# Kernel optimization log

Hardware: AMD Instinct MI355X
Metric: run time of the kernel (lower is better)

## Reference

```python
import jax, jax.numpy as jnp
import numpy as np

B, C, H, W = 8, 256, 64, 64
NH = 8
CM = 2048
EPS = 1e-5


def setup_inputs() -> dict:
    key = jax.random.key(0)
    ks = jax.random.split(key, 16)
    n = lambda k, s: (jax.random.normal(k, s, dtype=jnp.float32) * 0.02)
    return {
        'x': jax.random.normal(ks[0], (B, C, H, W), dtype=jnp.float32),
        'Wqkv': n(ks[1], (C, 3 * C)), 'bqkv': n(ks[2], (3 * C,)),
        'dw_w': n(ks[3], (C, 1, 3, 3)), 'dw_b': n(ks[4], (C,)),
        'Wproj': n(ks[5], (C, C)), 'bproj': n(ks[6], (C,)),
        'bn1_g': jnp.ones((C,), jnp.float32), 'bn1_b': jnp.zeros((C,), jnp.float32),
        'bn1_m': n(ks[7], (C,)), 'bn1_v': jax.random.uniform(ks[8], (C,), dtype=jnp.float32) + 0.5,
        'alpha1': jnp.ones((1,), jnp.float32),
        'Wfc1': n(ks[9], (C, CM)), 'bfc1': n(ks[10], (CM,)),
        'Wfc2': n(ks[11], (CM, C)), 'bfc2': n(ks[12], (C,)),
        'bn2_g': jnp.ones((C,), jnp.float32), 'bn2_b': jnp.zeros((C,), jnp.float32),
        'bn2_m': n(ks[13], (C,)), 'bn2_v': jax.random.uniform(ks[14], (C,), dtype=jnp.float32) + 0.5,
        'alpha2': jnp.ones((1,), jnp.float32),
    }


def _repbn(x, g, b, m, v, alpha):
    # eval-mode RepBN: BatchNorm1d with running stats over channel dim + alpha*x
    bn = (x - m) * jax.lax.rsqrt(v + EPS) * g + b
    return bn + alpha * x


def reference(x, Wqkv, bqkv, dw_w, dw_b, Wproj, bproj,
              bn1_g, bn1_b, bn1_m, bn1_v, alpha1,
              Wfc1, bfc1, Wfc2, bfc2,
              bn2_g, bn2_b, bn2_m, bn2_v, alpha2):
    b, c, h, w = x.shape
    n = h * w
    hd = c // NH
    scale = hd ** (-0.5)
    t = x.reshape(b, c, n).transpose(0, 2, 1)  # [B,N,C]

    # --- SimplifiedLinearAttention ---
    qkv = (t @ Wqkv + bqkv).reshape(b, n, 3, NH, hd).transpose(2, 0, 3, 1, 4)
    q, k, v = qkv[0], qkv[1], qkv[2]          # [B,H,N,hd]
    q = jax.nn.relu(q) * scale
    k = jax.nn.relu(k)
    ctx = jnp.einsum('bhnd,bhne->bhde', k, v)  # [B,H,hd,hd] small context
    out = jnp.einsum('bhnd,bhde->bhne', q, ctx)
    out = out.transpose(0, 2, 1, 3).reshape(b, n, c)
    img = out.transpose(0, 2, 1).reshape(b, c, h, w)
    img = jax.lax.conv_general_dilated(img, dw_w, (1, 1), 'SAME',
                                       feature_group_count=c)
    img = img + dw_b[None, :, None, None]
    out = img.reshape(b, c, n).transpose(0, 2, 1)
    out = out @ Wproj + bproj

    # residual + RepBN (eval branch of LinearNorm)
    t = _repbn(t + out, bn1_g, bn1_b, bn1_m, bn1_v, alpha1)

    # FFN (exact GELU as nn.GELU default)
    ff = jax.nn.gelu(t @ Wfc1 + bfc1, approximate=False) @ Wfc2 + bfc2
    t = _repbn(t + ff, bn2_g, bn2_b, bn2_m, bn2_v, alpha2)

    return t.transpose(0, 2, 1).reshape(b, c, h, w)
```

## Files before the change

### kernel.cpp

```cpp
#include <hip/hip_runtime.h>
#include <hip/hip_bf16.h>
#include <math.h>

constexpr int B_ = 8, C_ = 256, H_ = 64, W_ = 64;
constexpr int N_ = H_ * W_;
constexpr int NH_ = 8;
constexpr int CM_ = 2048;
constexpr int M_ = B_ * N_;
constexpr float EPS_ = 1e-5f;

typedef __bf16 bf16_t;
typedef bf16_t bf16x8 __attribute__((ext_vector_type(8)));
typedef float f32x4 __attribute__((ext_vector_type(4)));

__device__ inline bf16_t f2b(float f) {
    __hip_bfloat16 h = __float2bfloat16(f);
    return *reinterpret_cast<bf16_t*>(&h);
}
__device__ inline float b2f(bf16_t b) {
    unsigned short u = *reinterpret_cast<unsigned short*>(&b);
    unsigned int x = (unsigned int)u << 16;
    return *reinterpret_cast<float*>(&x);
}

#define GLOAD_LDS16(gptr, lptr)                                                     \
    __builtin_amdgcn_global_load_lds(                                               \
        (const __attribute__((address_space(1))) void*)(gptr),                      \
        (__attribute__((address_space(3))) void*)(lptr), 16, 0, 0)

template <int MODE>
__global__ void transpose_cast(const void* __restrict__ in_, bf16_t* __restrict__ outb) {
    __shared__ float tile[32][33];
    int b  = blockIdx.z;
    int n0 = blockIdx.x * 32;
    int c0 = blockIdx.y * 32;
    int tx = threadIdx.x, ty = threadIdx.y;
#pragma unroll
    for (int i = ty; i < 32; i += 8) {
        size_t off = (size_t)b * C_ * N_ + (size_t)(c0 + i) * N_ + n0 + tx;
        tile[i][tx] = (MODE == 0) ? ((const float*)in_)[off] : b2f(((const bf16_t*)in_)[off]);
    }
    __syncthreads();
#pragma unroll
    for (int i = ty; i < 32; i += 8) {
        size_t off = (size_t)b * N_ * C_ + (size_t)(n0 + i) * C_ + c0 + tx;
        outb[off] = f2b(tile[tx][i]);
    }
}

__global__ void wcastT(const float* __restrict__ W, bf16_t* __restrict__ Wt,
                       int K, int N) {
    __shared__ float tile[32][33];
    int k0 = blockIdx.y * 32, n0 = blockIdx.x * 32;
    int tx = threadIdx.x, ty = threadIdx.y;
#pragma unroll
    for (int i = ty; i < 32; i += 8)
        tile[i][tx] = W[(size_t)(k0 + i) * N + n0 + tx];
    __syncthreads();
#pragma unroll
    for (int i = ty; i < 32; i += 8)
        Wt[(size_t)(n0 + i) * K + k0 + tx] = f2b(tile[tx][i]);
}

template <int EPI>
__global__ __launch_bounds__(256)
void gemm_bf16(const bf16_t* __restrict__ A, const bf16_t* __restrict__ Bt,
               const float* __restrict__ bias,
               float* __restrict__ Cf, bf16_t* __restrict__ Cb,
               int M, int N, int K,
               const bf16_t* __restrict__ tres_b,
               const float* __restrict__ g, const float* __restrict__ bb,
               const float* __restrict__ mm, const float* __restrict__ vv,
               const float* __restrict__ alpha, int row_off) {
    __shared__ bf16x8 ldsv[2048];
    char* lds = (char*)ldsv;

    int tid  = threadIdx.x;
    int lane = tid & 63;
    int w    = tid >> 6;
    int wm   = w >> 1, wn = w & 1;
    int brow = blockIdx.y * 128, bcol = blockIdx.x * 128;
    int rowl = lane & 15, kq = lane >> 4;

    f32x4 acc[4][4] = {};

    for (int k0 = 0; k0 < K; k0 += 64) {
#pragma unroll
        for (int j = 0; j < 4; ++j) {
            int jj = w * 4 + j;
            int msub = jj >> 1, kh = jj & 1;
            const bf16_t* ga = A + ((size_t)(brow + msub * 16 + rowl) * K + k0 + kh * 32 + kq * 8);
            GLOAD_LDS16(ga, lds + jj * 1024);
            const bf16_t* gb = Bt + ((size_t)(bcol + msub * 16 + rowl) * K + k0 + kh * 32 + kq * 8);
            GLOAD_LDS16(gb, lds + 16384 + jj * 1024);
        }
        __syncthreads();
#pragma unroll
        for (int ks = 0; ks < 2; ++ks) {
            bf16x8 af[4], bfr[4];
#pragma unroll
            for (int m = 0; m < 4; ++m) af[m] = ldsv[((wm * 4 + m) * 2 + ks) * 64 + lane];
#pragma unroll
            for (int n = 0; n < 4; ++n) bfr[n] = ldsv[1024 + ((wn * 4 + n) * 2 + ks) * 64 + lane];
#pragma unroll
            for (int m = 0; m < 4; ++m)
#pragma unroll
                for (int n = 0; n < 4; ++n)
                    acc[m][n] = __builtin_amdgcn_mfma_f32_16x16x32_bf16(af[m], bfr[n], acc[m][n], 0, 0, 0);
        }
        __syncthreads();
    }

    float alpha_v = (EPI == 1 || EPI == 3) ? alpha[0] : 0.f;
#pragma unroll
    for (int m = 0; m < 4; ++m) {
#pragma unroll
        for (int n = 0; n < 4; ++n) {
            int col = bcol + wn * 64 + n * 16 + (lane & 15);
            float bv = bias[col];
#pragma unroll
            for (int r = 0; r < 4; ++r) {
                int row = brow + wm * 64 + m * 16 + (lane >> 4) * 4 + r;
                float y = acc[m][n][r] + bv;
                if (EPI == 4) {
                    Cb[(size_t)row * N + col] = f2b(y);
                } else if (EPI == 2) {
                    float u = y * (0.7978845608f + 0.0356774081f * y * y);
                    float e = __expf(2.0f * u);
                    float ge = y - y * __builtin_amdgcn_rcpf(e + 1.0f);
                    Cb[(size_t)row * N + col] = f2b(ge);
                } else if (EPI == 1) {
                    float z = b2f(tres_b[(size_t)row * N + col]) + y;
                    float rr = (z - mm[col]) * rsqrtf(vv[col] + EPS_) * g[col] + bb[col] + alpha_v * z;
                    Cb[(size_t)row * N + col] = f2b(rr);
                } else {
                    int grow = row_off + row;
                    float z = b2f(tres_b[(size_t)grow * C_ + col]) + y;
                    float rr = (z - mm[col]) * rsqrtf(vv[col] + EPS_) * g[col] + bb[col] + alpha_v * z;
                    int bi = grow >> 12, ni = grow & (N_ - 1);
                    Cf[((size_t)bi * C_ + col) * N_ + ni] = rr;
                }
            }
        }
    }
}

__global__ void ctx_partial(const bf16_t* __restrict__ qkv, float* __restrict__ ctxp) {
    __shared__ float kb[64][40];
    __shared__ float vb[64][40];
    int seg = blockIdx.x;
    int bh  = blockIdx.y;
    int b = bh >> 3, h = bh & 7;
    int tid = threadIdx.x;
    int d  = tid >> 3;
    int e0 = (tid & 7) * 4;
    int lrow = tid >> 2, lcol = (tid & 3) * 8;
    float acc[4] = {0.f, 0.f, 0.f, 0.f};
    const size_t base = (size_t)b * N_ * 768 + h * 32;
    for (int n0 = seg * 512; n0 < seg * 512 + 512; n0 += 64) {
        size_t ra = base + (size_t)(n0 + lrow) * 768 + lcol;
        bf16x8 kv8 = *(const bf16x8*)(qkv + ra + 256);
        bf16x8 vv8 = *(const bf16x8*)(qkv + ra + 512);
#pragma unroll
        for (int j = 0; j < 8; ++j) {
            kb[lrow][lcol + j] = b2f(kv8[j]);
            vb[lrow][lcol + j] = b2f(vv8[j]);
        }
        __syncthreads();
#pragma unroll
        for (int nl = 0; nl < 64; ++nl) {
            float kv = fmaxf(kb[nl][d], 0.f);
#pragma unroll
            for (int j = 0; j < 4; ++j)
                acc[j] = fmaf(kv, vb[nl][e0 + j], acc[j]);
        }
        __syncthreads();
    }
    float* o = ctxp + ((size_t)seg * 64 + bh) * 1024 + d * 32 + e0;
#pragma unroll
    for (int j = 0; j < 4; ++j) o[j] = acc[j];
}

__global__ void ctx_reduce(const float* __restrict__ ctxp, float* __restrict__ ctx) {
    int idx = blockIdx.x * 256 + threadIdx.x;
    float s = 0.f;
#pragma unroll
    for (int seg = 0; seg < 8; ++seg) s += ctxp[(size_t)seg * 65536 + idx];
    ctx[idx] = s;
}

__global__ void attn_out(const bf16_t* __restrict__ qkv, const float* __restrict__ ctx,
                         bf16_t* __restrict__ img) {
    __shared__ float qb[64][33];
    __shared__ float cs[32][32];
    int n0 = blockIdx.x * 64;
    int bh = blockIdx.y;
    int b = bh >> 3, h = bh & 7;
    int tid = threadIdx.x;
    const float scale = 0.17677669529663687f;
    {
        float4 vv = ((const float4*)(ctx + (size_t)bh * 1024))[tid];
        ((float4*)&cs[0][0])[tid] = vv;
    }
    const size_t base = (size_t)b * N_ * 768 + h * 32;
    int lrow = tid >> 2, lcol = (tid & 3) * 8;
    {
        bf16x8 q8 = *(const bf16x8*)(qkv + base + (size_t)(n0 + lrow) * 768 + lcol);
#pragma unroll
        for (int j = 0; j < 8; ++j)
            qb[lrow][lcol + j] = fmaxf(b2f(q8[j]), 0.f) * scale;
    }
    __syncthreads();
    int nl = tid & 63, ebase = tid >> 6;
    bf16_t* outp = img + ((size_t)b * C_ + h * 32) * N_ + n0 + nl;
#pragma unroll
    for (int p = 0; p < 8; ++p) {
        int e = ebase + p * 4;
        float s = 0.f;
#pragma unroll
        for (int dd = 0; dd < 32; ++dd)
            s = fmaf(qb[nl][dd], cs[dd][e], s);
        outp[(size_t)e * N_] = f2b(s);
    }
}

__global__ __launch_bounds__(256)
void dwconv3x3(const bf16_t* __restrict__ img, const float* __restrict__ w,
               const float* __restrict__ bias, bf16_t* __restrict__ out) {
    __shared__ float sp[64][65];
    int bc = blockIdx.x;
    int c  = bc & 255;
    int tid = threadIdx.x;
    const bf16_t* ip = img + (size_t)bc * N_;
#pragma unroll
    for (int l = 0; l < 2; ++l) {
        int flat = (tid + l * 256) * 8;
        int row = flat >> 6, col = flat & 63;
        bf16x8 v8 = *(const bf16x8*)(ip + flat);
#pragma unroll
        for (int j = 0; j < 8; ++j) sp[row][col + j] = b2f(v8[j]);
    }
    float wv[9];
#pragma unroll
    for (int j = 0; j < 9; ++j) wv[j] = w[c * 9 + j];
    float bv = bias[c];
    __syncthreads();

    int y = tid >> 2, x0 = (tid & 3) * 16;
    float o[16];
#pragma unroll
    for (int i = 0; i < 16; ++i) o[i] = bv;
#pragma unroll
    for (int dy = -1; dy <= 1; ++dy) {
        int yy = y + dy;
        if (yy < 0 || yy > 63) continue;
#pragma unroll
        for (int dx = -1; dx <= 1; ++dx) {
            float wgt = wv[(dy + 1) * 3 + dx + 1];
#pragma unroll
            for (int i = 0; i < 16; ++i) {
                int xx = x0 + i + dx;
                float val = (xx < 0 || xx > 63) ? 0.f : sp[yy][xx];
                o[i] = fmaf(wgt, val, o[i]);
            }
        }
    }
    bf16_t ob[16];
#pragma unroll
    for (int i = 0; i < 16; ++i) ob[i] = f2b(o[i]);
    *(bf16x8*)(out + (size_t)bc * N_ + y * 64 + x0)     = *(bf16x8*)&ob[0];
    *(bf16x8*)(out + (size_t)bc * N_ + y * 64 + x0 + 8) = *(bf16x8*)&ob[8];
}

extern "C" void kernel_launch(void* const* d_in, const int* in_sizes, int n_in,
                              void* d_out, int out_size, void* d_ws, size_t ws_size,
                              hipStream_t stream) {
    const float* x     = (const float*)d_in[0];
    const float* Wqkv  = (const float*)d_in[1];
    const float* bqkv  = (const float*)d_in[2];
    const float* dw_w  = (const float*)d_in[3];
    const float* dw_b  = (const float*)d_in[4];
    const float* Wproj = (const float*)d_in[5];
    const float* bproj = (const float*)d_in[6];
    const float* bn1_g = (const float*)d_in[7];
    const float* bn1_b = (const float*)d_in[8];
    const float* bn1_m = (const float*)d_in[9];
    const float* bn1_v = (const float*)d_in[10];
    const float* alpha1= (const float*)d_in[11];
    const float* Wfc1  = (const float*)d_in[12];
    const float* bfc1  = (const float*)d_in[13];
    const float* Wfc2  = (const float*)d_in[14];
    const float* bfc2  = (const float*)d_in[15];
    const float* bn2_g = (const float*)d_in[16];
    const float* bn2_b = (const float*)d_in[17];
    const float* bn2_m = (const float*)d_in[18];
    const float* bn2_v = (const float*)d_in[19];
    const float* alpha2= (const float*)d_in[20];
    float* out = (float*)d_out;

    char* ws = (char*)d_ws;
    bf16_t* t_b2    = (bf16_t*)(ws);
    bf16_t* WqkvT   = (bf16_t*)(ws + 16777216);
    bf16_t* WprojT  = (bf16_t*)(ws + 17170432);
    bf16_t* Wfc1T   = (bf16_t*)(ws + 17301504);
    bf16_t* Wfc2T   = (bf16_t*)(ws + 18350080);
    float*  ctxp    = (float*)(ws + 19398656);
    float*  ctx     = (float*)(ws + 21495808);
    bf16_t* t_b     = (bf16_t*)(ws + 21757952);
    bf16_t* qkv_b   = (bf16_t*)(ws + 38535168);
    bf16_t* img_b   = (bf16_t*)(ws + 88866816);
    bf16_t* conv_b  = (bf16_t*)(ws + 105644032);
    bf16_t* convT_b = (bf16_t*)(ws + 122421248);
    bf16_t* hidden  = (bf16_t*)(ws + 21757952);

    transpose_cast<0><<<dim3(N_ / 32, C_ / 32, B_), dim3(32, 8), 0, stream>>>(x, t_b);
    wcastT<<<dim3(768 / 32, C_ / 32), dim3(32, 8), 0, stream>>>(Wqkv, WqkvT, C_, 768);
    wcastT<<<dim3(C_ / 32, C_ / 32), dim3(32, 8), 0, stream>>>(Wproj, WprojT, C_, C_);
    wcastT<<<dim3(CM_ / 32, C_ / 32), dim3(32, 8), 0, stream>>>(Wfc1, Wfc1T, C_, CM_);
    wcastT<<<dim3(C_ / 32, CM_ / 32), dim3(32, 8), 0, stream>>>(Wfc2, Wfc2T, CM_, C_);

    gemm_bf16<4><<<dim3(768 / 128, M_ / 128), 256, 0, stream>>>(
        t_b, WqkvT, bqkv, nullptr, qkv_b, M_, 768, C_,
        nullptr, nullptr, nullptr, nullptr, nullptr, nullptr, 0);

    ctx_partial<<<dim3(8, B_ * NH_), 256, 0, stream>>>(qkv_b, ctxp);
    ctx_reduce<<<256, 256, 0, stream>>>(ctxp, ctx);

    attn_out<<<dim3(N_ / 64, B_ * NH_), 256, 0, stream>>>(qkv_b, ctx, img_b);

    dwconv3x3<<<B_ * C_, 256, 0, stream>>>(img_b, dw_w, dw_b, conv_b);

    transpose_cast<1><<<dim3(N_ / 32, C_ / 32, B_), dim3(32, 8), 0, stream>>>(conv_b, convT_b);

    gemm_bf16<1><<<dim3(C_ / 128, M_ / 128), 256, 0, stream>>>(
        convT_b, WprojT, bproj, nullptr, t_b2, M_, C_, C_,
        t_b, bn1_g, bn1_b, bn1_m, bn1_v, alpha1, 0);

    gemm_bf16<2><<<dim3(CM_ / 128, M_ / 128), 256, 0, stream>>>(
        t_b2, Wfc1T, bfc1, nullptr, hidden, M_, CM_, C_,
        nullptr, nullptr, nullptr, nullptr, nullptr, nullptr, 0);

    gemm_bf16<3><<<dim3(C_ / 128, M_ / 128), 256, 0, stream>>>(
        hidden, Wfc2T, bfc2, out, nullptr, M_, C_, CM_,
        t_b2, bn2_g, bn2_b, bn2_m, bn2_v, alpha2, 0);
}
```

Before: 349.8 us.

## Fuse FFN fc1+GELU+fc2+RepBN into one kernel keeping hidden on-chip

Replaces the separate fc1 (GELU epilogue) and fc2 (RepBN epilogue) GEMMs with a single kernel in which each block holds 128 rows of activations in registers. The kernel streams 32-column chunks of W1 and W2 through double-buffered LDS, computes the GELU hidden chunk with 32x32 MFMAs, repacks it through lane shuffles and accumulates fc2 directly. This is meant to remove the 64 MB bf16 hidden tensor round trip through HBM and one launch. In exchange, grid size drops to 256 blocks, each block uses 128 KB of LDS so occupancy is low, and weights are reloaded per block with a sync on every chunk.

```diff
diff --git a/kernel.cpp b/kernel.cpp
--- a/kernel.cpp
+++ b/kernel.cpp
@@ -12,6 +12,8 @@
 typedef __bf16 bf16_t;
 typedef bf16_t bf16x8 __attribute__((ext_vector_type(8)));
 typedef float f32x4 __attribute__((ext_vector_type(4)));
+typedef float f32x16 __attribute__((ext_vector_type(16)));
+typedef unsigned int u32x4 __attribute__((ext_vector_type(4)));
 
 __device__ inline bf16_t f2b(float f) {
     __hip_bfloat16 h = __float2bfloat16(f);
@@ -21,6 +23,17 @@
     unsigned short u = *reinterpret_cast<unsigned short*>(&b);
     unsigned int x = (unsigned int)u << 16;
     return *reinterpret_cast<float*>(&x);
+}
+__device__ inline unsigned pk2(float lo, float hi) {
+    bf16_t l = f2b(lo), h = f2b(hi);
+    unsigned short ls = *reinterpret_cast<unsigned short*>(&l);
+    unsigned short hs = *reinterpret_cast<unsigned short*>(&h);
+    return ((unsigned)hs << 16) | (unsigned)ls;
+}
+__device__ inline float gelu_ap(float y) {
+    float u = y * (0.7978845608f + 0.0356774081f * y * y);
+    float e = __expf(2.0f * u);
+    return y - y * __builtin_amdgcn_rcpf(e + 1.0f);
 }
 
 #define GLOAD_LDS16(gptr, lptr)                                                     \
@@ -111,7 +124,7 @@
         __syncthreads();
     }
 
-    float alpha_v = (EPI == 1 || EPI == 3) ? alpha[0] : 0.f;
+    float alpha_v = (EPI == 1) ? alpha[0] : 0.f;
 #pragma unroll
     for (int m = 0; m < 4; ++m) {
 #pragma unroll
@@ -124,23 +137,138 @@
                 float y = acc[m][n][r] + bv;
                 if (EPI == 4) {
                     Cb[(size_t)row * N + col] = f2b(y);
-                } else if (EPI == 2) {
-                    float u = y * (0.7978845608f + 0.0356774081f * y * y);
-                    float e = __expf(2.0f * u);
-                    float ge = y - y * __builtin_amdgcn_rcpf(e + 1.0f);
-                    Cb[(size_t)row * N + col] = f2b(ge);
-                } else if (EPI == 1) {
+                } else {
                     float z = b2f(tres_b[(size_t)row * N + col]) + y;
                     float rr = (z - mm[col]) * rsqrtf(vv[col] + EPS_) * g[col] + bb[col] + alpha_v * z;
                     Cb[(size_t)row * N + col] = f2b(rr);
-                } else {
-                    int grow = row_off + row;
-                    float z = b2f(tres_b[(size_t)grow * C_ + col]) + y;
-                    float rr = (z - mm[col]) * rsqrtf(vv[col] + EPS_) * g[col] + bb[col] + alpha_v * z;
-                    int bi = grow >> 12, ni = grow & (N_ - 1);
-                    Cf[((size_t)bi * C_ + col) * N_ + ni] = rr;
                 }
             }
+        }
+    }
+}
+
+__global__ __launch_bounds__(256)
+void ffn_fused(const bf16_t* __restrict__ Aact, const bf16_t* __restrict__ W1t,
+               const bf16_t* __restrict__ W2t,
+               const float* __restrict__ bfc1, const float* __restrict__ bfc2,
+               const float* __restrict__ g, const float* __restrict__ bb,
+               const float* __restrict__ mm, const float* __restrict__ vv,
+               const float* __restrict__ alpha, float* __restrict__ out) {
+    __shared__ bf16x8 ldsv[8192];
+    char* lds = (char*)ldsv;
+    const int tid = threadIdx.x;
+    const int lane = tid & 63;
+    const int w = tid >> 6;
+    const int l31 = lane & 31;
+    const int h = lane >> 5;
+    const int brow = blockIdx.x * 128;
+
+    {
+        const bf16_t* ga = Aact + (size_t)(brow + 32 * w + l31) * 256 + h * 8;
+#pragma unroll
+        for (int kc = 0; kc < 16; ++kc)
+            GLOAD_LDS16(ga + kc * 16, lds + (w * 16 + kc) * 1024);
+        const bf16_t* g1 = W1t + (size_t)l31 * 256 + h * 8;
+#pragma unroll
+        for (int i = 0; i < 4; ++i) {
+            int kc = w * 4 + i;
+            GLOAD_LDS16(g1 + kc * 16, lds + 65536 + kc * 1024);
+        }
+#pragma unroll
+        for (int i = 0; i < 4; ++i) {
+            int fid = w * 4 + i, cb = fid >> 1, ks = fid & 1;
+            const bf16_t* g2 = W2t + (size_t)(32 * cb + l31) * 2048 + ks * 16 + h * 8;
+            GLOAD_LDS16(g2, lds + 98304 + fid * 1024);
+        }
+    }
+    __syncthreads();
+
+    bf16x8 areg[16];
+#pragma unroll
+    for (int kc = 0; kc < 16; ++kc) areg[kc] = ldsv[(w * 16 + kc) * 64 + lane];
+
+    f32x16 acc2[8];
+#pragma unroll
+    for (int cb = 0; cb < 8; ++cb) acc2[cb] = (f32x16)0.f;
+
+    const float* bp1 = bfc1 + 4 * h;
+
+    for (int c = 0; c < 64; ++c) {
+        int p = c & 1;
+        if (c + 1 < 64) {
+            int cn = c + 1, pn = p ^ 1;
+            const bf16_t* g1 = W1t + (size_t)(32 * cn + l31) * 256 + h * 8;
+#pragma unroll
+            for (int i = 0; i < 4; ++i) {
+                int kc = w * 4 + i;
+                GLOAD_LDS16(g1 + kc * 16, lds + 65536 + pn * 16384 + kc * 1024);
+            }
+#pragma unroll
+            for (int i = 0; i < 4; ++i) {
+                int fid = w * 4 + i, cb = fid >> 1, ks = fid & 1;
+                const bf16_t* g2 = W2t + (size_t)(32 * cb + l31) * 2048 + 32 * cn + ks * 16 + h * 8;
+                GLOAD_LDS16(g2, lds + 98304 + pn * 16384 + fid * 1024);
+            }
+        }
+
+        f32x16 acc1;
+#pragma unroll
+        for (int r = 0; r < 16; ++r)
+            acc1[r] = bp1[32 * c + (r & 3) + 8 * (r >> 2)];
+#pragma unroll
+        for (int kc = 0; kc < 16; ++kc) {
+            bf16x8 w1f = ldsv[4096 + p * 1024 + kc * 64 + lane];
+            acc1 = __builtin_amdgcn_mfma_f32_32x32x16_bf16(w1f, areg[kc], acc1, 0, 0, 0);
+        }
+
+        unsigned words[8];
+#pragma unroll
+        for (int t = 0; t < 4; ++t)
+#pragma unroll
+            for (int s = 0; s < 2; ++s)
+                words[t * 2 + s] = pk2(gelu_ap(acc1[4 * t + 2 * s]),
+                                       gelu_ap(acc1[4 * t + 2 * s + 1]));
+        bf16x8 hf[2];
+#pragma unroll
+        for (int ks = 0; ks < 2; ++ks) {
+            unsigned u0 = words[(2 * ks) * 2 + 0], u1 = words[(2 * ks) * 2 + 1];
+            unsigned v0 = words[(2 * ks + 1) * 2 + 0], v1 = words[(2 * ks + 1) * 2 + 1];
+            unsigned su0 = __shfl_xor(u0, 32);
+            unsigned su1 = __shfl_xor(u1, 32);
+            unsigned sv0 = __shfl_xor(v0, 32);
+            unsigned sv1 = __shfl_xor(v1, 32);
+            u32x4 t4;
+            t4[0] = h ? sv0 : u0;
+            t4[1] = h ? sv1 : u1;
+            t4[2] = h ? v0 : su0;
+            t4[3] = h ? v1 : su1;
+            hf[ks] = __builtin_bit_cast(bf16x8, t4);
+        }
+
+#pragma unroll
+        for (int cb = 0; cb < 8; ++cb) {
+            bf16x8 w2f0 = ldsv[6144 + p * 1024 + (cb * 2 + 0) * 64 + lane];
+            acc2[cb] = __builtin_amdgcn_mfma_f32_32x32x16_bf16(hf[0], w2f0, acc2[cb], 0, 0, 0);
+            bf16x8 w2f1 = ldsv[6144 + p * 1024 + (cb * 2 + 1) * 64 + lane];
+            acc2[cb] = __builtin_amdgcn_mfma_f32_32x32x16_bf16(hf[1], w2f1, acc2[cb], 0, 0, 0);
+        }
+        __syncthreads();
+    }
+
+    float alpha_v = alpha[0];
+#pragma unroll
+    for (int cb = 0; cb < 8; ++cb) {
+        int cc = cb * 32 + l31;
+        float bv = bfc2[cc];
+        float rs = rsqrtf(vv[cc] + EPS_) * g[cc];
+        float bbv = bb[cc], mv = mm[cc];
+#pragma unroll
+        for (int r = 0; r < 16; ++r) {
+            int m = brow + 32 * w + (r & 3) + 8 * (r >> 2) + 4 * h;
+            float z = b2f(Aact[(size_t)m * 256 + cc]) + acc2[cb][r] + bv;
+            float rr = (z - mv) * rs + bbv + alpha_v * z;
+            int bi = m >> 12, ni = m & (N_ - 1);
+            out[((size_t)bi * C_ + cc) * N_ + ni] = rr;
         }
     }
 }
@@ -311,7 +439,6 @@
     bf16_t* img_b   = (bf16_t*)(ws + 88866816);
     bf16_t* conv_b  = (bf16_t*)(ws + 105644032);
     bf16_t* convT_b = (bf16_t*)(ws + 122421248);
-    bf16_t* hidden  = (bf16_t*)(ws + 21757952);
 
     transpose_cast<0><<<dim3(N_ / 32, C_ / 32, B_), dim3(32, 8), 0, stream>>>(x, t_b);
     wcastT<<<dim3(768 / 32, C_ / 32), dim3(32, 8), 0, stream>>>(Wqkv, WqkvT, C_, 768);
@@ -336,11 +463,7 @@
         convT_b, WprojT, bproj, nullptr, t_b2, M_, C_, C_,
         t_b, bn1_g, bn1_b, bn1_m, bn1_v, alpha1, 0);
 
-    gemm_bf16<2><<<dim3(CM_ / 128, M_ / 128), 256, 0, stream>>>(
-        t_b2, Wfc1T, bfc1, nullptr, hidden, M_, CM_, C_,
-        nullptr, nullptr, nullptr, nullptr, nullptr, nullptr, 0);
-
-    gemm_bf16<3><<<dim3(C_ / 128, M_ / 128), 256, 0, stream>>>(
-        hidden, Wfc2T, bfc2, out, nullptr, M_, C_, CM_,
-        t_b2, bn2_g, bn2_b, bn2_m, bn2_v, alpha2, 0);
-}
+    ffn_fused<<<M_ / 128, 256, 0, stream>>>(
+        t_b2, Wfc1T, Wfc2T, bfc1, bfc2,
+        bn2_g, bn2_b, bn2_m, bn2_v, alpha2, out);
+}
```

New measurement: 377.9 us. 8.0% more time.

## Stage GEMM epilogue through LDS for vectorized stores and swizzle block order

Applied to the files above, without the earlier changes.

Rewrites the GEMM epilogue so bf16-output variants stage accumulators in a per-wave XOR-swizzled LDS buffer and write eight contiguous bf16 values per lane with vector loads of bias and BN parameters. The fp32 transposed-output variant writes four consecutive spatial positions per store instead of scalar scattered writes. It also remaps block indices with a stride-8 swizzle to change which tiles run together for L2 reuse. This targets uncoalesced 2-byte scattered stores in the epilogues, at the cost of LDS round-trips and reliance on explicit waitcnt ordering within each wave.

```diff
diff --git a/kernel.cpp b/kernel.cpp
--- a/kernel.cpp
+++ b/kernel.cpp
@@ -21,6 +21,11 @@
     unsigned short u = *reinterpret_cast<unsigned short*>(&b);
     unsigned int x = (unsigned int)u << 16;
     return *reinterpret_cast<float*>(&x);
+}
+__device__ inline float gelu_ap(float y) {
+    float u = y * (0.7978845608f + 0.0356774081f * y * y);
+    float e = __expf(2.0f * u);
+    return y - y * __builtin_amdgcn_rcpf(e + 1.0f);
 }
 
 #define GLOAD_LDS16(gptr, lptr)                                                     \
@@ -71,7 +76,7 @@
                const bf16_t* __restrict__ tres_b,
                const float* __restrict__ g, const float* __restrict__ bb,
                const float* __restrict__ mm, const float* __restrict__ vv,
-               const float* __restrict__ alpha, int row_off) {
+               const float* __restrict__ alpha) {
     __shared__ bf16x8 ldsv[2048];
     char* lds = (char*)ldsv;
 
@@ -79,7 +84,13 @@
     int lane = tid & 63;
     int w    = tid >> 6;
     int wm   = w >> 1, wn = w & 1;
-    int brow = blockIdx.y * 128, bcol = blockIdx.x * 128;
+
+    int nwg = gridDim.x * gridDim.y;
+    int bid = blockIdx.y * gridDim.x + blockIdx.x;
+    int swz = (bid & 7) * (nwg >> 3) + (bid >> 3);
+    int bx = swz % gridDim.x, by = swz / gridDim.x;
+    int brow = by * 128, bcol = bx * 128;
+
     int rowl = lane & 15, kq = lane >> 4;
 
     f32x4 acc[4][4] = {};
@@ -112,34 +123,86 @@
     }
 
     float alpha_v = (EPI == 1 || EPI == 3) ? alpha[0] : 0.f;
-#pragma unroll
-    for (int m = 0; m < 4; ++m) {
-#pragma unroll
-        for (int n = 0; n < 4; ++n) {
-            int col = bcol + wn * 64 + n * 16 + (lane & 15);
-            float bv = bias[col];
-#pragma unroll
-            for (int r = 0; r < 4; ++r) {
-                int row = brow + wm * 64 + m * 16 + (lane >> 4) * 4 + r;
-                float y = acc[m][n][r] + bv;
+
+    if (EPI == 3) {
+#pragma unroll
+        for (int m = 0; m < 4; ++m) {
+            int mbase = brow + wm * 64 + m * 16 + (lane >> 4) * 4;
+            int bi = mbase >> 12, ni = mbase & (N_ - 1);
+#pragma unroll
+            for (int n = 0; n < 4; ++n) {
+                int col = bcol + wn * 64 + n * 16 + (lane & 15);
+                float bv = bias[col];
+                float rs = rsqrtf(vv[col] + EPS_) * g[col];
+                float bbv = bb[col], mv = mm[col];
+                f32x4 o4;
+#pragma unroll
+                for (int r = 0; r < 4; ++r) {
+                    float z = b2f(tres_b[(size_t)(mbase + r) * C_ + col]) + acc[m][n][r] + bv;
+                    o4[r] = (z - mv) * rs + bbv + alpha_v * z;
+                }
+                *(f32x4*)(Cf + ((size_t)bi * C_ + col) * N_ + ni) = o4;
+            }
+        }
+    } else {
+        float* fl = (float*)ldsv + w * 2048;
+        const int c8 = lane & 7, rbase = (lane >> 3) * 4;
+#pragma unroll
+        for (int half = 0; half < 2; ++half) {
+            if (half)
+                asm volatile("s_waitcnt lgkmcnt(0)" ::: "memory");
+#pragma unroll
+            for (int m2 = 0; m2 < 2; ++m2) {
+                int m = half * 2 + m2;
+#pragma unroll
+                for (int n = 0; n < 4; ++n)
+#pragma unroll
+                    for (int r = 0; r < 4; ++r) {
+                        int rl = m2 * 16 + (lane >> 4) * 4 + r;
+                        int cl = n * 16 + (lane & 15);
+                        int scl = cl ^ (((rl >> 2) & 3) << 4);
+                        fl[rl * 64 + scl] = acc[m][n][r];
+                    }
+            }
+            asm volatile("s_waitcnt lgkmcnt(0)" ::: "memory");
+#pragma unroll
+            for (int rr = 0; rr < 4; ++rr) {
+                int rl = rbase + rr;
+                int xr = ((rl >> 2) & 3) << 4;
+                f32x4 lo = *(f32x4*)&fl[rl * 64 + ((c8 * 8) ^ xr)];
+                f32x4 hi = *(f32x4*)&fl[rl * 64 + ((c8 * 8 + 4) ^ xr)];
+                int grow = brow + wm * 64 + half * 32 + rl;
+                int gcol = bcol + wn * 64 + c8 * 8;
+                f32x4 b0 = *(const f32x4*)(bias + gcol);
+                f32x4 b1 = *(const f32x4*)(bias + gcol + 4);
+                float y[8];
+#pragma unroll
+                for (int j = 0; j < 4; ++j) { y[j] = lo[j] + b0[j]; y[4 + j] = hi[j] + b1[j]; }
+                bf16_t ob[8];
                 if (EPI == 4) {
-                    Cb[(size_t)row * N + col] = f2b(y);
+#pragma unroll
+                    for (int j = 0; j < 8; ++j) ob[j] = f2b(y[j]);
                 } else if (EPI == 2) {
-                    float u = y * (0.7978845608f + 0.0356774081f * y * y);
-                    float e = __expf(2.0f * u);
-                    float ge = y - y * __builtin_amdgcn_rcpf(e + 1.0f);
-                    Cb[(size_t)row * N + col] = f2b(ge);
-                } else if (EPI == 1) {
-                    float z = b2f(tres_b[(size_t)row * N + col]) + y;
-                    float rr = (z - mm[col]) * rsqrtf(vv[col] + EPS_) * g[col] + bb[col] + alpha_v * z;
-                    Cb[(size_t)row * N + col] = f2b(rr);
+#pragma unroll
+                    for (int j = 0; j < 8; ++j) ob[j] = f2b(gelu_ap(y[j]));
                 } else {
-                    int grow = row_off + row;
-                    float z = b2f(tres_b[(size_t)grow * C_ + col]) + y;
-                    float rr = (z - mm[col]) * rsqrtf(vv[col] + EPS_) * g[col] + bb[col] + alpha_v * z;
-                    int bi = grow >> 12, ni = grow & (N_ - 1);
-                    Cf[((size_t)bi * C_ + col) * N_ + ni] = rr;
+                    bf16x8 t8 = *(const bf16x8*)(tres_b + (size_t)grow * N + gcol);
+                    f32x4 g0 = *(const f32x4*)(g + gcol),  g1 = *(const f32x4*)(g + gcol + 4);
+                    f32x4 B0 = *(const f32x4*)(bb + gcol), B1 = *(const f32x4*)(bb + gcol + 4);
+                    f32x4 m0 = *(const f32x4*)(mm + gcol), m1 = *(const f32x4*)(mm + gcol + 4);
+                    f32x4 v0 = *(const f32x4*)(vv + gcol), v1 = *(const f32x4*)(vv + gcol + 4);
+#pragma unroll
+                    for (int j = 0; j < 8; ++j) {
+                        float gv = j < 4 ? g0[j] : g1[j - 4];
+                        float bbv = j < 4 ? B0[j] : B1[j - 4];
+                        float mv = j < 4 ? m0[j] : m1[j - 4];
+                        float vr = j < 4 ? v0[j] : v1[j - 4];
+                        float z = b2f(t8[j]) + y[j];
+                        float r2 = (z - mv) * rsqrtf(vr + EPS_) * gv + bbv + alpha_v * z;
+                        ob[j] = f2b(r2);
+                    }
                 }
+                *(bf16x8*)(Cb + (size_t)grow * N + gcol) = *(bf16x8*)ob;
             }
         }
     }
@@ -321,7 +384,7 @@
 
     gemm_bf16<4><<<dim3(768 / 128, M_ / 128), 256, 0, stream>>>(
         t_b, WqkvT, bqkv, nullptr, qkv_b, M_, 768, C_,
-        nullptr, nullptr, nullptr, nullptr, nullptr, nullptr, 0);
+        nullptr, nullptr, nullptr, nullptr, nullptr, nullptr);
 
     ctx_partial<<<dim3(8, B_ * NH_), 256, 0, stream>>>(qkv_b, ctxp);
     ctx_reduce<<<256, 256, 0, stream>>>(ctxp, ctx);
@@ -334,13 +397,13 @@
 
     gemm_bf16<1><<<dim3(C_ / 128, M_ / 128), 256, 0, stream>>>(
         convT_b, WprojT, bproj, nullptr, t_b2, M_, C_, C_,
-        t_b, bn1_g, bn1_b, bn1_m, bn1_v, alpha1, 0);
+        t_b, bn1_g, bn1_b, bn1_m, bn1_v, alpha1);
 
     gemm_bf16<2><<<dim3(CM_ / 128, M_ / 128), 256, 0, stream>>>(
         t_b2, Wfc1T, bfc1, nullptr, hidden, M_, CM_, C_,
-        nullptr, nullptr, nullptr, nullptr, nullptr, nullptr, 0);
+        nullptr, nullptr, nullptr, nullptr, nullptr, nullptr);
 
     gemm_bf16<3><<<dim3(C_ / 128, M_ / 128), 256, 0, stream>>>(
         hidden, Wfc2T, bfc2, out, nullptr, M_, C_, CM_,
-        t_b2, bn2_g, bn2_b, bn2_m, bn2_v, alpha2, 0);
-}
+        t_b2, bn2_g, bn2_b, bn2_m, bn2_v, alpha2);
+}
```

Result: faster. 342.5 us (-2.1%).
